# Kernel tuning notes

Hardware: AMD Instinct MI355X
Metric: run time of the kernel (lower is better)

Reference implementation:

```python
import jax, jax.numpy as jnp
import numpy as np

B, D, H1, H2 = 512, 1024, 512, 128

def setup_inputs() -> dict:
    key = jax.random.key(0)
    ks = jax.random.split(key, 3)
    x = jax.random.normal(ks[0], (B, D), dtype=jnp.float32)
    W1 = jax.random.normal(ks[1], (H1, D), dtype=jnp.float32)
    W2 = jax.random.normal(ks[2], (H2, H1), dtype=jnp.float32)
    b1 = jnp.full((H1,), 0.1, dtype=jnp.float32)
    b2 = jnp.full((H2,), 0.1, dtype=jnp.float32)
    b3 = jnp.full((H1,), 0.1, dtype=jnp.float32)
    b_r = jnp.full((D,), 0.1, dtype=jnp.float32)
    return {"x": x, "W1": W1, "b1": b1, "W2": W2, "b2": b2, "b3": b3, "b_r": b_r}

def reference(x, W1, b1, W2, b2, b3, b_r):
    # encoder
    c1 = jax.nn.sigmoid(x @ W1.T + b1)          # [B, H1]
    c2 = jax.nn.sigmoid(c1 @ W2.T + b2)         # [B, H2]
    # decoder (tied weights)
    c3 = jax.nn.sigmoid(c2 @ W2 + b3)           # [B, H1]
    recover = c3 @ W1 + b_r                     # [B, D]
    # Jacobian of code w.r.t. x, batched (replaces per-sample diag+matmul loop):
    # Jac[b] = diag(c2'(b)) @ W2 @ diag(c1'(b)) @ W1
    s1p = c1 * (1.0 - c1)                       # [B, H1]
    s2p = c2 * (1.0 - c2)                       # [B, H2]
    M = s2p[:, :, None] * W2[None, :, :] * s1p[:, None, :]   # [B, H2, H1]
    Jac = jnp.einsum('bhk,kd->bhd', M, W1)      # [B, H2, D]
    return (recover, c2, Jac)
```

## Files before the change

### kernel.cpp

```cpp
#include <hip/hip_runtime.h>


typedef _Float16 f16x8 __attribute__((ext_vector_type(8)));
typedef _Float16 f16x4 __attribute__((ext_vector_type(4)));
typedef float    f32x4 __attribute__((ext_vector_type(4)));
typedef float    f32x2 __attribute__((ext_vector_type(2)));

__device__ __forceinline__ void gld_lds16(const _Float16* src, _Float16* dst_wave_uniform) {
    __builtin_amdgcn_global_load_lds((const __attribute__((address_space(1))) unsigned int*)src,
                                     (__attribute__((address_space(3))) unsigned int*)dst_wave_uniform,
                                     16, 0, 0);
}

__device__ __forceinline__ void prep_dev(int bx, const float* __restrict__ W1,
                                         const float* __restrict__ W2,
                                         _Float16* __restrict__ W1T,
                                         _Float16* __restrict__ W2h) {
    if (bx < 512) {
        __shared__ float tile[32][33];
        int dt = (bx & 31) * 32, kt = (bx >> 5) * 32;
        int tx = threadIdx.x & 31, ty = threadIdx.x >> 5;
        #pragma unroll
        for (int r = 0; r < 32; r += 8)
            tile[ty + r][tx] = W1[(kt + ty + r) * 1024 + dt + tx];
        __syncthreads();
        #pragma unroll
        for (int r = 0; r < 32; r += 8)
            W1T[(size_t)(dt + ty + r) * 512 + kt + tx] = (_Float16)tile[tx][ty + r];
    } else {
        int i = (bx - 512) * 1024 + threadIdx.x * 4;
        f32x4 v = *(const f32x4*)(W2 + i);
        f16x4 h;
        h.x = (_Float16)v.x; h.y = (_Float16)v.y; h.z = (_Float16)v.z; h.w = (_Float16)v.w;
        *(f16x4*)(W2h + i) = h;
    }
}

template <int EPI, bool TRANSB>
__device__ void gemm_dev(const float* __restrict__ A, const float* __restrict__ Bm,
                         const float* __restrict__ bias,
                         float* __restrict__ C, float* __restrict__ Cd,
                         _Float16* __restrict__ Ch,
                         int M, int N, int K, int m0, int n0) {
    __shared__ __align__(16) float As[32][34];
    __shared__ __align__(16) float Bs[32][68];
    const int tid = threadIdx.x, tx = tid & 15, ty = tid >> 4;
    const int ka  = tid & 31, ma  = tid >> 5;
    const int kbt = tid & 31, nbt = tid >> 5;
    const int nbf = tid & 63, kbf = tid >> 6;
    float acc[2][4] = {};
    float rA[4], rB[8];

    #pragma unroll
    for (int r = 0; r < 4; ++r) rA[r] = A[(size_t)(m0 + ma + 8 * r) * K + ka];
    if (TRANSB) {
        #pragma unroll
        for (int r = 0; r < 8; ++r) rB[r] = Bm[(size_t)(n0 + nbt + 8 * r) * K + kbt];
    } else {
        #pragma unroll
        for (int r = 0; r < 8; ++r) rB[r] = Bm[(size_t)(kbf + 4 * r) * N + n0 + nbf];
    }

    for (int k0 = 0; k0 < K; k0 += 32) {
        #pragma unroll
        for (int r = 0; r < 4; ++r) As[ka][ma + 8 * r] = rA[r];
        if (TRANSB) {
            #pragma unroll
            for (int r = 0; r < 8; ++r) Bs[kbt][nbt + 8 * r] = rB[r];
        } else {
            #pragma unroll
            for (int r = 0; r < 8; ++r) Bs[kbf + 4 * r][nbf] = rB[r];
        }
        const int k1 = k0 + 32;
        if (k1 < K) {
            #pragma unroll
            for (int r = 0; r < 4; ++r) rA[r] = A[(size_t)(m0 + ma + 8 * r) * K + k1 + ka];
            if (TRANSB) {
                #pragma unroll
                for (int r = 0; r < 8; ++r) rB[r] = Bm[(size_t)(n0 + nbt + 8 * r) * K + k1 + kbt];
            } else {
                #pragma unroll
                for (int r = 0; r < 8; ++r) rB[r] = Bm[(size_t)(k1 + kbf + 4 * r) * N + n0 + nbf];
            }
        }
        __syncthreads();
        #pragma unroll
        for (int k = 0; k < 32; ++k) {
            f32x2 av = *(const f32x2*)&As[k][ty * 2];
            f32x4 bv = *(const f32x4*)&Bs[k][tx * 4];
            #pragma unroll
            for (int i = 0; i < 2; ++i)
                #pragma unroll
                for (int j = 0; j < 4; ++j)
                    acc[i][j] += av[i] * bv[j];
        }
        __syncthreads();
    }

    #pragma unroll
    for (int i = 0; i < 2; ++i) {
        int row = m0 + ty * 2 + i;
        #pragma unroll
        for (int j = 0; j < 4; ++j) {
            int col = n0 + tx * 4 + j;
            float z = acc[i][j] + bias[col];
            float s = 1.f / (1.f + __expf(-z));
            if constexpr (EPI == 1) {
                C[(size_t)row * N + col]  = s;
                Cd[(size_t)row * N + col] = s * (1.f - s);
            } else {
                Ch[(size_t)row * N + col] = (_Float16)s;
            }
        }
    }
}

__global__ __launch_bounds__(256) void fused_prep_gemm1(const float* __restrict__ x,
                                                        const float* __restrict__ W1,
                                                        const float* __restrict__ b1,
                                                        const float* __restrict__ W2,
                                                        _Float16* __restrict__ W1T,
                                                        _Float16* __restrict__ W2h,
                                                        float* __restrict__ c1,
                                                        float* __restrict__ s1p) {
    int bx = blockIdx.x;
    if (bx < 128) {
        gemm_dev<1, true>(x, W1, b1, c1, s1p, nullptr, 512, 512, 1024,
                          (bx >> 3) * 32, (bx & 7) * 64);
    } else {
        prep_dev(bx - 128, W1, W2, W1T, W2h);
    }
}

__global__ __launch_bounds__(256) void gemm2_kernel(const float* __restrict__ c1,
                                                    const float* __restrict__ W2,
                                                    const float* __restrict__ b2,
                                                    float* __restrict__ out_c2,
                                                    float* __restrict__ s2p) {
    gemm_dev<1, true>(c1, W2, b2, out_c2, s2p, nullptr, 512, 128, 512,
                      blockIdx.y * 32, blockIdx.x * 64);
}

__global__ __launch_bounds__(256) void gemm3_kernel(const float* __restrict__ out_c2,
                                                    const float* __restrict__ W2,
                                                    const float* __restrict__ b3,
                                                    _Float16* __restrict__ c3h) {
    gemm_dev<2, false>(out_c2, W2, b3, nullptr, nullptr, c3h, 512, 512, 128,
                       (blockIdx.x >> 3) * 32, (blockIdx.x & 7) * 64);
}

__global__ __launch_bounds__(256, 2) void jacW_fused(const _Float16* __restrict__ c3h,
                                                     const _Float16* __restrict__ W2h,
                                                     const _Float16* __restrict__ W1T,
                                                     const float* __restrict__ s1p,
                                                     const float* __restrict__ s2p,
                                                     const float* __restrict__ br,
                                                     float* __restrict__ out_rec,
                                                     float* __restrict__ out_jac) {
    __shared__ __align__(16) _Float16 Wsl[128 * 64];
    __shared__ __align__(16) _Float16 Bsl[128 * 64];
    __shared__ _Float16 S1h[2][512];
    __shared__ float    S2s[2][128];

    const int tid = threadIdx.x;
    const int lane = tid & 63, wave = tid >> 6;
    const int wm = (wave >> 1) * 64, wn = (wave & 1) * 64;
    const int l15 = lane & 15, q = lane >> 4;
    const int bid = blockIdx.x;

    const int srow = wave * 8 + (lane >> 3);
    const int skof = ((lane & 7) ^ (lane >> 3)) * 8;

    if (bid < 32) {
        const int m0 = (bid >> 3) * 128, n0 = (bid & 7) * 128;
        const _Float16* Abase = c3h + (size_t)m0 * 512;
        const _Float16* Bbase = W1T + (size_t)n0 * 512;
        float* outp = out_rec + (size_t)m0 * 1024;
        if (tid < 128) S2s[0][tid] = br[n0 + tid];

        f32x4 acc[4][4];
        #pragma unroll
        for (int i = 0; i < 4; ++i)
            #pragma unroll
            for (int j = 0; j < 4; ++j) acc[i][j] = (f32x4){0.f, 0.f, 0.f, 0.f};

        for (int t = 0; t < 8; ++t) {
            const int kb = t * 64;
            #pragma unroll
            for (int r = 0; r < 4; ++r) {
                gld_lds16(Abase + (size_t)(r * 32 + srow) * 512 + kb + skof, Wsl + (r * 32 + wave * 8) * 64);
                gld_lds16(Bbase + (size_t)(r * 32 + srow) * 512 + kb + skof, Bsl + (r * 32 + wave * 8) * 64);
            }
            __syncthreads();
            #pragma unroll
            for (int kk = 0; kk < 64; kk += 32) {
                f16x8 af[4], bf[4];
                #pragma unroll
                for (int i = 0; i < 4; ++i)
                    af[i] = *(const f16x8*)(Wsl + (wm + i * 16 + l15) * 64 + ((kk + q * 8) ^ ((l15 & 7) * 8)));
                #pragma unroll
                for (int j = 0; j < 4; ++j)
                    bf[j] = *(const f16x8*)(Bsl + (wn + j * 16 + l15) * 64 + ((kk + q * 8) ^ ((l15 & 7) * 8)));
                #pragma unroll
                for (int i = 0; i < 4; ++i)
                    #pragma unroll
                    for (int j = 0; j < 4; ++j)
                        acc[i][j] = __builtin_amdgcn_mfma_f32_16x16x32_f16(af[i], bf[j], acc[i][j], 0, 0, 0);
            }
            __syncthreads();
        }

        #pragma unroll
        for (int i = 0; i < 4; ++i) {
            #pragma unroll
            for (int rg = 0; rg < 4; ++rg) {
                int ml = wm + i * 16 + q * 4 + rg;
                #pragma unroll
                for (int j = 0; j < 4; ++j) {
                    int cl = wn + j * 16 + l15;
                    __builtin_nontemporal_store(acc[i][j][rg] + S2s[0][cl],
                                                outp + (size_t)ml * 1024 + n0 + cl);
                }
            }
        }
        return;
    }

    const int jid = bid - 32;
    const int w = (jid & 7) * 256 + (jid >> 3);
    const int pair = w >> 3, n0 = (w & 7) * 128;
    const int bA = pair * 2;

    S1h[0][tid]       = (_Float16)s1p[(size_t)bA * 512 + tid];
    S1h[0][tid + 256] = (_Float16)s1p[(size_t)bA * 512 + 256 + tid];
    S1h[1][tid]       = (_Float16)s1p[(size_t)(bA + 1) * 512 + tid];
    S1h[1][tid + 256] = (_Float16)s1p[(size_t)(bA + 1) * 512 + 256 + tid];
    if (tid < 128) S2s[0][tid] = s2p[(size_t)bA * 128 + tid];
    else           S2s[1][tid - 128] = s2p[(size_t)(bA + 1) * 128 + (tid - 128)];

    const _Float16* Bbase = W1T + (size_t)n0 * 512;

    f32x4 accA[4][4], accB[4][4];
    #pragma unroll
    for (int i = 0; i < 4; ++i)
        #pragma unroll
        for (int j = 0; j < 4; ++j) {
            accA[i][j] = (f32x4){0.f, 0.f, 0.f, 0.f};
            accB[i][j] = (f32x4){0.f, 0.f, 0.f, 0.f};
        }

    for (int t = 0; t < 8; ++t) {
        const int kb = t * 64;
        #pragma unroll
        for (int r = 0; r < 4; ++r) {
            gld_lds16(W2h   + (size_t)(r * 32 + srow) * 512 + kb + skof, Wsl + (r * 32 + wave * 8) * 64);
            gld_lds16(Bbase + (size_t)(r * 32 + srow) * 512 + kb + skof, Bsl + (r * 32 + wave * 8) * 64);
        }
        __syncthreads();
        #pragma unroll
        for (int kk = 0; kk < 64; kk += 32) {
            const f16x8 sfA = *(const f16x8*)(&S1h[0][kb + kk + q * 8]);
            const f16x8 sfB = *(const f16x8*)(&S1h[1][kb + kk + q * 8]);
            f16x8 bf[4];
            #pragma unroll
            for (int j = 0; j < 4; ++j)
                bf[j] = *(const f16x8*)(Bsl + (wn + j * 16 + l15) * 64 + ((kk + q * 8) ^ ((l15 & 7) * 8)));
            #pragma unroll
            for (int i = 0; i < 4; ++i) {
                const f16x8 wf = *(const f16x8*)(Wsl + (wm + i * 16 + l15) * 64 + ((kk + q * 8) ^ ((l15 & 7) * 8)));
                f16x8 af = wf * sfA;
                #pragma unroll
                for (int j = 0; j < 4; ++j)
                    accA[i][j] = __builtin_amdgcn_mfma_f32_16x16x32_f16(af, bf[j], accA[i][j], 0, 0, 0);
                af = wf * sfB;
                #pragma unroll
                for (int j = 0; j < 4; ++j)
                    accB[i][j] = __builtin_amdgcn_mfma_f32_16x16x32_f16(af, bf[j], accB[i][j], 0, 0, 0);
            }
        }
        __syncthreads();
    }

    float* outA = out_jac + (size_t)bA * (128 * 1024);
    float* outB = outA + (128 * 1024);
    #pragma unroll
    for (int i = 0; i < 4; ++i) {
        #pragma unroll
        for (int rg = 0; rg < 4; ++rg) {
            int ml = wm + i * 16 + q * 4 + rg;
            float rsA = S2s[0][ml], rsB = S2s[1][ml];
            #pragma unroll
            for (int j = 0; j < 4; ++j) {
                int cl = wn + j * 16 + l15;
                __builtin_nontemporal_store(accA[i][j][rg] * rsA, outA + (size_t)ml * 1024 + n0 + cl);
                __builtin_nontemporal_store(accB[i][j][rg] * rsB, outB + (size_t)ml * 1024 + n0 + cl);
            }
        }
    }
}

extern "C" void kernel_launch(void* const* d_in, const int* in_sizes, int n_in,
                              void* d_out, int out_size, void* d_ws, size_t ws_size,
                              hipStream_t stream) {
    const float* x  = (const float*)d_in[0];
    const float* W1 = (const float*)d_in[1];
    const float* b1 = (const float*)d_in[2];
    const float* W2 = (const float*)d_in[3];
    const float* b2 = (const float*)d_in[4];
    const float* b3 = (const float*)d_in[5];
    const float* br = (const float*)d_in[6];

    float* out_rec = (float*)d_out;
    float* out_c2  = out_rec + 512 * 1024;
    float* out_jac = out_c2 + 512 * 128;

    char* ws = (char*)d_ws;
    _Float16* W1T = (_Float16*)(ws);
    _Float16* W2h = (_Float16*)(ws + 0x100000);
    float*    c1  = (float*)(ws + 0x120000);
    float*    s1p = (float*)(ws + 0x220000);
    float*    s2p = (float*)(ws + 0x320000);
    _Float16* c3h = (_Float16*)(ws + 0x360000);

    fused_prep_gemm1<<<704, 256, 0, stream>>>(x, W1, b1, W2, W1T, W2h, c1, s1p);
    gemm2_kernel<<<dim3(2, 16), 256, 0, stream>>>(c1, W2, b2, out_c2, s2p);
    gemm3_kernel<<<128, 256, 0, stream>>>(out_c2, W2, b3, c3h);
    jacW_fused<<<2080, 256, 0, stream>>>(c3h, W2h, W1T, s1p, s2p, br, out_rec, out_jac);
}
```

Baseline: 404.3 us.

## Split paired-sample Jacobian GEMM into two passes, overlapping first sample's stores

The Jacobian block previously computed both samples of a pair in one K loop and stored everything at the end. Now it computes sample A fully, then streams sample A's output stores in slices interleaved with sample B's K-loop iterations, so global writes overlap MFMA work. The cost is loading the W2 and W1T tiles into LDS twice (once per sample) and full unrolling of both loops, which increases code size and may change register pressure.

New measurement: 435.1 us. +7.6%, slower.

```diff
diff --git a/kernel.cpp b/kernel.cpp
--- a/kernel.cpp
+++ b/kernel.cpp
@@ -239,6 +239,8 @@
     else           S2s[1][tid - 128] = s2p[(size_t)(bA + 1) * 128 + (tid - 128)];
 
     const _Float16* Bbase = W1T + (size_t)n0 * 512;
+    float* outA = out_jac + (size_t)bA * (128 * 1024);
+    float* outB = outA + (128 * 1024);
 
     f32x4 accA[4][4], accB[4][4];
     #pragma unroll
@@ -249,6 +251,7 @@
             accB[i][j] = (f32x4){0.f, 0.f, 0.f, 0.f};
         }
 
+    #pragma unroll
     for (int t = 0; t < 8; ++t) {
         const int kb = t * 64;
         #pragma unroll
@@ -260,6 +263,48 @@
         #pragma unroll
         for (int kk = 0; kk < 64; kk += 32) {
             const f16x8 sfA = *(const f16x8*)(&S1h[0][kb + kk + q * 8]);
+            f16x8 bf[4];
+            #pragma unroll
+            for (int j = 0; j < 4; ++j)
+                bf[j] = *(const f16x8*)(Bsl + (wn + j * 16 + l15) * 64 + ((kk + q * 8) ^ ((l15 & 7) * 8)));
+            #pragma unroll
+            for (int i = 0; i < 4; ++i) {
+                const f16x8 wf = *(const f16x8*)(Wsl + (wm + i * 16 + l15) * 64 + ((kk + q * 8) ^ ((l15 & 7) * 8)));
+                const f16x8 af = wf * sfA;
+                #pragma unroll
+                for (int j = 0; j < 4; ++j)
+                    accA[i][j] = __builtin_amdgcn_mfma_f32_16x16x32_f16(af, bf[j], accA[i][j], 0, 0, 0);
+            }
+        }
+        __syncthreads();
+    }
+
+    #pragma unroll
+    for (int t = 0; t < 8; ++t) {
+        const int kb = t * 64;
+        #pragma unroll
+        for (int r = 0; r < 4; ++r) {
+            gld_lds16(W2h   + (size_t)(r * 32 + srow) * 512 + kb + skof, Wsl + (r * 32 + wave * 8) * 64);
+            gld_lds16(Bbase + (size_t)(r * 32 + srow) * 512 + kb + skof, Bsl + (r * 32 + wave * 8) * 64);
+        }
+        {
+            const int i = t >> 1;
+            #pragma unroll
+            for (int r2 = 0; r2 < 2; ++r2) {
+                const int rg = (t & 1) * 2 + r2;
+                const int ml = wm + i * 16 + q * 4 + rg;
+                const float rs = S2s[0][ml];
+                #pragma unroll
+                for (int j = 0; j < 4; ++j) {
+                    const int cl = wn + j * 16 + l15;
+                    __builtin_nontemporal_store(accA[i][j][rg] * rs,
+                                                outA + (size_t)ml * 1024 + n0 + cl);
+                }
+            }
+        }
+        __syncthreads();
+        #pragma unroll
+        for (int kk = 0; kk < 64; kk += 32) {
             const f16x8 sfB = *(const f16x8*)(&S1h[1][kb + kk + q * 8]);
             f16x8 bf[4];
             #pragma unroll
@@ -268,11 +313,7 @@
             #pragma unroll
             for (int i = 0; i < 4; ++i) {
                 const f16x8 wf = *(const f16x8*)(Wsl + (wm + i * 16 + l15) * 64 + ((kk + q * 8) ^ ((l15 & 7) * 8)));
-                f16x8 af = wf * sfA;
-                #pragma unroll
-                for (int j = 0; j < 4; ++j)
-                    accA[i][j] = __builtin_amdgcn_mfma_f32_16x16x32_f16(af, bf[j], accA[i][j], 0, 0, 0);
-                af = wf * sfB;
+                const f16x8 af = wf * sfB;
                 #pragma unroll
                 for (int j = 0; j < 4; ++j)
                     accB[i][j] = __builtin_amdgcn_mfma_f32_16x16x32_f16(af, bf[j], accB[i][j], 0, 0, 0);
@@ -281,19 +322,17 @@
         __syncthreads();
     }
 
-    float* outA = out_jac + (size_t)bA * (128 * 1024);
-    float* outB = outA + (128 * 1024);
     #pragma unroll
     for (int i = 0; i < 4; ++i) {
         #pragma unroll
         for (int rg = 0; rg < 4; ++rg) {
-            int ml = wm + i * 16 + q * 4 + rg;
-            float rsA = S2s[0][ml], rsB = S2s[1][ml];
+            const int ml = wm + i * 16 + q * 4 + rg;
+            const float rs = S2s[1][ml];
             #pragma unroll
             for (int j = 0; j < 4; ++j) {
-                int cl = wn + j * 16 + l15;
-                __builtin_nontemporal_store(accA[i][j][rg] * rsA, outA + (size_t)ml * 1024 + n0 + cl);
-                __builtin_nontemporal_store(accB[i][j][rg] * rsB, outB + (size_t)ml * 1024 + n0 + cl);
+                const int cl = wn + j * 16 + l15;
+                __builtin_nontemporal_store(accB[i][j][rg] * rs,
+                                            outB + (size_t)ml * 1024 + n0 + cl);
             }
         }
     }
```

## Merge four launches into one cooperative persistent kernel with grid syncs

Applied to the files above, without the earlier changes.

Replaces the four separate kernel launches with a single cooperative mega-kernel of 512 blocks that runs prep/GEMM1, GEMM2, GEMM3 and the Jacobian/recover phase separated by grid-wide syncs, with a persistent loop over the 2080 final-phase work units. The goal is to remove launch gaps and inter-kernel drain/fill overhead. The cost is grid.sync latency, fixed 512-block occupancy (launch bounds of 2 blocks per CU), loss of the earlier interleaved jac work ordering for L2 reuse, and the early GEMM phases running on few blocks. Falls back to the old path if cooperative launch fails.

After: 574.5 us. +42.1%, slower.

```diff
diff --git a/kernel.cpp b/kernel.cpp
--- a/kernel.cpp
+++ b/kernel.cpp
@@ -1,4 +1,7 @@
 #include <hip/hip_runtime.h>
+#include <hip/hip_cooperative_groups.h>
+
+namespace cg = cooperative_groups;
 
 
 typedef _Float16 f16x8 __attribute__((ext_vector_type(8)));
@@ -20,6 +23,7 @@
         __shared__ float tile[32][33];
         int dt = (bx & 31) * 32, kt = (bx >> 5) * 32;
         int tx = threadIdx.x & 31, ty = threadIdx.x >> 5;
+        __syncthreads();
         #pragma unroll
         for (int r = 0; r < 32; r += 8)
             tile[ty + r][tx] = W1[(kt + ty + r) * 1024 + dt + tx];
@@ -115,6 +119,206 @@
     }
 }
 
+__device__ __forceinline__ void unit_guard() {
+    asm volatile("s_waitcnt lgkmcnt(0)" ::: "memory");
+    __builtin_amdgcn_sched_barrier(0);
+    __builtin_amdgcn_s_barrier();
+}
+
+__device__ __forceinline__ void recover_unit(int u,
+        _Float16* __restrict__ Wsl, _Float16* __restrict__ Bsl, float* __restrict__ S2s0,
+        const _Float16* __restrict__ c3h, const _Float16* __restrict__ W1T,
+        const float* __restrict__ br, float* __restrict__ out_rec) {
+    const int tid = threadIdx.x;
+    const int lane = tid & 63, wave = tid >> 6;
+    const int wm = (wave >> 1) * 64, wn = (wave & 1) * 64;
+    const int l15 = lane & 15, q = lane >> 4;
+    const int srow = wave * 8 + (lane >> 3);
+    const int skof = ((lane & 7) ^ (lane >> 3)) * 8;
+
+    unit_guard();
+
+    const int m0 = (u >> 3) * 128, n0 = (u & 7) * 128;
+    const _Float16* Abase = c3h + (size_t)m0 * 512;
+    const _Float16* Bbase = W1T + (size_t)n0 * 512;
+    float* outp = out_rec + (size_t)m0 * 1024;
+    if (tid < 128) S2s0[tid] = br[n0 + tid];
+
+    f32x4 acc[4][4];
+    #pragma unroll
+    for (int i = 0; i < 4; ++i)
+        #pragma unroll
+        for (int j = 0; j < 4; ++j) acc[i][j] = (f32x4){0.f, 0.f, 0.f, 0.f};
+
+    for (int t = 0; t < 8; ++t) {
+        const int kb = t * 64;
+        #pragma unroll
+        for (int r = 0; r < 4; ++r) {
+            gld_lds16(Abase + (size_t)(r * 32 + srow) * 512 + kb + skof, Wsl + (r * 32 + wave * 8) * 64);
+            gld_lds16(Bbase + (size_t)(r * 32 + srow) * 512 + kb + skof, Bsl + (r * 32 + wave * 8) * 64);
+        }
+        __syncthreads();
+        #pragma unroll
+        for (int kk = 0; kk < 64; kk += 32) {
+            f16x8 af[4], bf[4];
+            #pragma unroll
+            for (int i = 0; i < 4; ++i)
+                af[i] = *(const f16x8*)(Wsl + (wm + i * 16 + l15) * 64 + ((kk + q * 8) ^ ((l15 & 7) * 8)));
+            #pragma unroll
+            for (int j = 0; j < 4; ++j)
+                bf[j] = *(const f16x8*)(Bsl + (wn + j * 16 + l15) * 64 + ((kk + q * 8) ^ ((l15 & 7) * 8)));
+            #pragma unroll
+            for (int i = 0; i < 4; ++i)
+                #pragma unroll
+                for (int j = 0; j < 4; ++j)
+                    acc[i][j] = __builtin_amdgcn_mfma_f32_16x16x32_f16(af[i], bf[j], acc[i][j], 0, 0, 0);
+        }
+        __syncthreads();
+    }
+
+    #pragma unroll
+    for (int i = 0; i < 4; ++i) {
+        #pragma unroll
+        for (int rg = 0; rg < 4; ++rg) {
+            int ml = wm + i * 16 + q * 4 + rg;
+            #pragma unroll
+            for (int j = 0; j < 4; ++j) {
+                int cl = wn + j * 16 + l15;
+                __builtin_nontemporal_store(acc[i][j][rg] + S2s0[cl],
+                                            outp + (size_t)ml * 1024 + n0 + cl);
+            }
+        }
+    }
+}
+
+__device__ __forceinline__ void jac_unit(int jid,
+        _Float16* __restrict__ Wsl, _Float16* __restrict__ Bsl,
+        _Float16 (*__restrict__ S1h)[512], float (*__restrict__ S2s)[128],
+        const _Float16* __restrict__ W2h, const _Float16* __restrict__ W1T,
+        const float* __restrict__ s1p, const float* __restrict__ s2p,
+        float* __restrict__ out_jac) {
+    const int tid = threadIdx.x;
+    const int lane = tid & 63, wave = tid >> 6;
+    const int wm = (wave >> 1) * 64, wn = (wave & 1) * 64;
+    const int l15 = lane & 15, q = lane >> 4;
+    const int srow = wave * 8 + (lane >> 3);
+    const int skof = ((lane & 7) ^ (lane >> 3)) * 8;
+
+    unit_guard();
+
+    const int pair = jid >> 3, n0 = (jid & 7) * 128;
+    const int bA = pair * 2;
+
+    S1h[0][tid]       = (_Float16)s1p[(size_t)bA * 512 + tid];
+    S1h[0][tid + 256] = (_Float16)s1p[(size_t)bA * 512 + 256 + tid];
+    S1h[1][tid]       = (_Float16)s1p[(size_t)(bA + 1) * 512 + tid];
+    S1h[1][tid + 256] = (_Float16)s1p[(size_t)(bA + 1) * 512 + 256 + tid];
+    if (tid < 128) S2s[0][tid] = s2p[(size_t)bA * 128 + tid];
+    else           S2s[1][tid - 128] = s2p[(size_t)(bA + 1) * 128 + (tid - 128)];
+
+    const _Float16* Bbase = W1T + (size_t)n0 * 512;
+
+    f32x4 accA[4][4], accB[4][4];
+    #pragma unroll
+    for (int i = 0; i < 4; ++i)
+        #pragma unroll
+        for (int j = 0; j < 4; ++j) {
+            accA[i][j] = (f32x4){0.f, 0.f, 0.f, 0.f};
+            accB[i][j] = (f32x4){0.f, 0.f, 0.f, 0.f};
+        }
+
+    for (int t = 0; t < 8; ++t) {
+        const int kb = t * 64;
+        #pragma unroll
+        for (int r = 0; r < 4; ++r) {
+            gld_lds16(W2h   + (size_t)(r * 32 + srow) * 512 + kb + skof, Wsl + (r * 32 + wave * 8) * 64);
+            gld_lds16(Bbase + (size_t)(r * 32 + srow) * 512 + kb + skof, Bsl + (r * 32 + wave * 8) * 64);
+        }
+        __syncthreads();
+        #pragma unroll
+        for (int kk = 0; kk < 64; kk += 32) {
+            const f16x8 sfA = *(const f16x8*)(&S1h[0][kb + kk + q * 8]);
+            const f16x8 sfB = *(const f16x8*)(&S1h[1][kb + kk + q * 8]);
+            f16x8 bf[4];
+            #pragma unroll
+            for (int j = 0; j < 4; ++j)
+                bf[j] = *(const f16x8*)(Bsl + (wn + j * 16 + l15) * 64 + ((kk + q * 8) ^ ((l15 & 7) * 8)));
+            #pragma unroll
+            for (int i = 0; i < 4; ++i) {
+                const f16x8 wf = *(const f16x8*)(Wsl + (wm + i * 16 + l15) * 64 + ((kk + q * 8) ^ ((l15 & 7) * 8)));
+                f16x8 af = wf * sfA;
+                #pragma unroll
+                for (int j = 0; j < 4; ++j)
+                    accA[i][j] = __builtin_amdgcn_mfma_f32_16x16x32_f16(af, bf[j], accA[i][j], 0, 0, 0);
+                af = wf * sfB;
+                #pragma unroll
+                for (int j = 0; j < 4; ++j)
+                    accB[i][j] = __builtin_amdgcn_mfma_f32_16x16x32_f16(af, bf[j], accB[i][j], 0, 0, 0);
+            }
+        }
+        __syncthreads();
+    }
+
+    float* outA = out_jac + (size_t)bA * (128 * 1024);
+    float* outB = outA + (128 * 1024);
+    #pragma unroll
+    for (int i = 0; i < 4; ++i) {
+        #pragma unroll
+        for (int rg = 0; rg < 4; ++rg) {
+            int ml = wm + i * 16 + q * 4 + rg;
+            float rsA = S2s[0][ml], rsB = S2s[1][ml];
+            #pragma unroll
+            for (int j = 0; j < 4; ++j) {
+                int cl = wn + j * 16 + l15;
+                __builtin_nontemporal_store(accA[i][j][rg] * rsA, outA + (size_t)ml * 1024 + n0 + cl);
+                __builtin_nontemporal_store(accB[i][j][rg] * rsB, outB + (size_t)ml * 1024 + n0 + cl);
+            }
+        }
+    }
+}
+
+__global__ __launch_bounds__(256, 2) void mega_kernel(
+        const float* __restrict__ x,  const float* __restrict__ W1, const float* __restrict__ b1,
+        const float* __restrict__ W2, const float* __restrict__ b2, const float* __restrict__ b3,
+        const float* __restrict__ br,
+        _Float16* __restrict__ W1T, _Float16* __restrict__ W2h,
+        float* __restrict__ c1, float* __restrict__ s1p, float* __restrict__ s2p,
+        _Float16* __restrict__ c3h,
+        float* __restrict__ out_rec, float* __restrict__ out_c2, float* __restrict__ out_jac) {
+    __shared__ __align__(16) _Float16 Wsl[128 * 64];
+    __shared__ __align__(16) _Float16 Bsl[128 * 64];
+    __shared__ _Float16 S1h[2][512];
+    __shared__ float    S2s[2][128];
+
+    cg::grid_group grid = cg::this_grid();
+    const int bid = blockIdx.x;
+
+    if (bid < 128) {
+        gemm_dev<1, true>(x, W1, b1, c1, s1p, nullptr, 512, 512, 1024,
+                          (bid >> 3) * 32, (bid & 7) * 64);
+    } else {
+        int u = bid - 128;
+        prep_dev(u, W1, W2, W1T, W2h);
+        if (u + 384 < 576) prep_dev(u + 384, W1, W2, W1T, W2h);
+    }
+    grid.sync();
+
+    if (bid < 32)
+        gemm_dev<1, true>(c1, W2, b2, out_c2, s2p, nullptr, 512, 128, 512,
+                          (bid >> 1) * 32, (bid & 1) * 64);
+    grid.sync();
+
+    if (bid < 128)
+        gemm_dev<2, false>(out_c2, W2, b3, nullptr, nullptr, c3h, 512, 512, 128,
+                           (bid >> 3) * 32, (bid & 7) * 64);
+    grid.sync();
+
+    for (int u = bid; u < 2080; u += 512) {
+        if (u < 32) recover_unit(u, Wsl, Bsl, S2s[0], c3h, W1T, br, out_rec);
+        else        jac_unit(u - 32, Wsl, Bsl, S1h, S2s, W2h, W1T, s1p, s2p, out_jac);
+    }
+}
+
 __global__ __launch_bounds__(256) void fused_prep_gemm1(const float* __restrict__ x,
                                                         const float* __restrict__ W1,
                                                         const float* __restrict__ b1,
@@ -162,141 +366,14 @@
     __shared__ _Float16 S1h[2][512];
     __shared__ float    S2s[2][128];
 
-    const int tid = threadIdx.x;
-    const int lane = tid & 63, wave = tid >> 6;
-    const int wm = (wave >> 1) * 64, wn = (wave & 1) * 64;
-    const int l15 = lane & 15, q = lane >> 4;
     const int bid = blockIdx.x;
-
-    const int srow = wave * 8 + (lane >> 3);
-    const int skof = ((lane & 7) ^ (lane >> 3)) * 8;
-
     if (bid < 32) {
-        const int m0 = (bid >> 3) * 128, n0 = (bid & 7) * 128;
-        const _Float16* Abase = c3h + (size_t)m0 * 512;
-        const _Float16* Bbase = W1T + (size_t)n0 * 512;
-        float* outp = out_rec + (size_t)m0 * 1024;
-        if (tid < 128) S2s[0][tid] = br[n0 + tid];
-
-        f32x4 acc[4][4];
-        #pragma unroll
-        for (int i = 0; i < 4; ++i)
-            #pragma unroll
-            for (int j = 0; j < 4; ++j) acc[i][j] = (f32x4){0.f, 0.f, 0.f, 0.f};
-
-        for (int t = 0; t < 8; ++t) {
-            const int kb = t * 64;
-            #pragma unroll
-            for (int r = 0; r < 4; ++r) {
-                gld_lds16(Abase + (size_t)(r * 32 + srow) * 512 + kb + skof, Wsl + (r * 32 + wave * 8) * 64);
-                gld_lds16(Bbase + (size_t)(r * 32 + srow) * 512 + kb + skof, Bsl + (r * 32 + wave * 8) * 64);
-            }
-            __syncthreads();
-            #pragma unroll
-            for (int kk = 0; kk < 64; kk += 32) {
-                f16x8 af[4], bf[4];
-                #pragma unroll
-                for (int i = 0; i < 4; ++i)
-                    af[i] = *(const f16x8*)(Wsl + (wm + i * 16 + l15) * 64 + ((kk + q * 8) ^ ((l15 & 7) * 8)));
-                #pragma unroll
-                for (int j = 0; j < 4; ++j)
-                    bf[j] = *(const f16x8*)(Bsl + (wn + j * 16 + l15) * 64 + ((kk + q * 8) ^ ((l15 & 7) * 8)));
-                #pragma unroll
-                for (int i = 0; i < 4; ++i)
-                    #pragma unroll
-                    for (int j = 0; j < 4; ++j)
-                        acc[i][j] = __builtin_amdgcn_mfma_f32_16x16x32_f16(af[i], bf[j], acc[i][j], 0, 0, 0);
-            }
-            __syncthreads();
-        }
-
-        #pragma unroll
-        for (int i = 0; i < 4; ++i) {
-            #pragma unroll
-            for (int rg = 0; rg < 4; ++rg) {
-                int ml = wm + i * 16 + q * 4 + rg;
-                #pragma unroll
-                for (int j = 0; j < 4; ++j) {
-                    int cl = wn + j * 16 + l15;
-                    __builtin_nontemporal_store(acc[i][j][rg] + S2s[0][cl],
-                                                outp + (size_t)ml * 1024 + n0 + cl);
-                }
-            }
-        }
+        recover_unit(bid, Wsl, Bsl, S2s[0], c3h, W1T, br, out_rec);
         return;
     }
-
     const int jid = bid - 32;
     const int w = (jid & 7) * 256 + (jid >> 3);
-    const int pair = w >> 3, n0 = (w & 7) * 128;
-    const int bA = pair * 2;
-
-    S1h[0][tid]       = (_Float16)s1p[(size_t)bA * 512 + tid];
-    S1h[0][tid + 256] = (_Float16)s1p[(size_t)bA * 512 + 256 + tid];
-    S1h[1][tid]       = (_Float16)s1p[(size_t)(bA + 1) * 512 + tid];
-    S1h[1][tid + 256] = (_Float16)s1p[(size_t)(bA + 1) * 512 + 256 + tid];
-    if (tid < 128) S2s[0][tid] = s2p[(size_t)bA * 128 + tid];
-    else           S2s[1][tid - 128] = s2p[(size_t)(bA + 1) * 128 + (tid - 128)];
-
-    const _Float16* Bbase = W1T + (size_t)n0 * 512;
-
-    f32x4 accA[4][4], accB[4][4];
-    #pragma unroll
-    for (int i = 0; i < 4; ++i)
-        #pragma unroll
-        for (int j = 0; j < 4; ++j) {
-            accA[i][j] = (f32x4){0.f, 0.f, 0.f, 0.f};
-            accB[i][j] = (f32x4){0.f, 0.f, 0.f, 0.f};
-        }
-
-    for (int t = 0; t < 8; ++t) {
-        const int kb = t * 64;
-        #pragma unroll
-        for (int r = 0; r < 4; ++r) {
-            gld_lds16(W2h   + (size_t)(r * 32 + srow) * 512 + kb + skof, Wsl + (r * 32 + wave * 8) * 64);
-            gld_lds16(Bbase + (size_t)(r * 32 + srow) * 512 + kb + skof, Bsl + (r * 32 + wave * 8) * 64);
-        }
-        __syncthreads();
-        #pragma unroll
-        for (int kk = 0; kk < 64; kk += 32) {
-            const f16x8 sfA = *(const f16x8*)(&S1h[0][kb + kk + q * 8]);
-            const f16x8 sfB = *(const f16x8*)(&S1h[1][kb + kk + q * 8]);
-            f16x8 bf[4];
-            #pragma unroll
-            for (int j = 0; j < 4; ++j)
-                bf[j] = *(const f16x8*)(Bsl + (wn + j * 16 + l15) * 64 + ((kk + q * 8) ^ ((l15 & 7) * 8)));
-            #pragma unroll
-            for (int i = 0; i < 4; ++i) {
-                const f16x8 wf = *(const f16x8*)(Wsl + (wm + i * 16 + l15) * 64 + ((kk + q * 8) ^ ((l15 & 7) * 8)));
-                f16x8 af = wf * sfA;
-                #pragma unroll
-                for (int j = 0; j < 4; ++j)
-                    accA[i][j] = __builtin_amdgcn_mfma_f32_16x16x32_f16(af, bf[j], accA[i][j], 0, 0, 0);
-                af = wf * sfB;
-                #pragma unroll
-                for (int j = 0; j < 4; ++j)
-                    accB[i][j] = __builtin_amdgcn_mfma_f32_16x16x32_f16(af, bf[j], accB[i][j], 0, 0, 0);
-            }
-        }
-        __syncthreads();
-    }
-
-    float* outA = out_jac + (size_t)bA * (128 * 1024);
-    float* outB = outA + (128 * 1024);
-    #pragma unroll
-    for (int i = 0; i < 4; ++i) {
-        #pragma unroll
-        for (int rg = 0; rg < 4; ++rg) {
-            int ml = wm + i * 16 + q * 4 + rg;
-            float rsA = S2s[0][ml], rsB = S2s[1][ml];
-            #pragma unroll
-            for (int j = 0; j < 4; ++j) {
-                int cl = wn + j * 16 + l15;
-                __builtin_nontemporal_store(accA[i][j][rg] * rsA, outA + (size_t)ml * 1024 + n0 + cl);
-                __builtin_nontemporal_store(accB[i][j][rg] * rsB, outB + (size_t)ml * 1024 + n0 + cl);
-            }
-        }
-    }
+    jac_unit(w, Wsl, Bsl, S1h, S2s, W2h, W1T, s1p, s2p, out_jac);
 }
 
 extern "C" void kernel_launch(void* const* d_in, const int* in_sizes, int n_in,
@@ -322,8 +399,24 @@
     float*    s2p = (float*)(ws + 0x320000);
     _Float16* c3h = (_Float16*)(ws + 0x360000);
 
-    fused_prep_gemm1<<<704, 256, 0, stream>>>(x, W1, b1, W2, W1T, W2h, c1, s1p);
-    gemm2_kernel<<<dim3(2, 16), 256, 0, stream>>>(c1, W2, b2, out_c2, s2p);
-    gemm3_kernel<<<128, 256, 0, stream>>>(out_c2, W2, b3, c3h);
-    jacW_fused<<<2080, 256, 0, stream>>>(c3h, W2h, W1T, s1p, s2p, br, out_rec, out_jac);
-}
+    int dev = 0, coop = 0;
+    hipGetDevice(&dev);
+    hipDeviceGetAttribute(&coop, hipDeviceAttributeCooperativeLaunch, dev);
+
+    hipError_t lerr = hipErrorUnknown;
+    if (coop) {
+        void* args[] = {(void*)&x, (void*)&W1, (void*)&b1, (void*)&W2, (void*)&b2,
+                        (void*)&b3, (void*)&br, (void*)&W1T, (void*)&W2h, (void*)&c1,
+                        (void*)&s1p, (void*)&s2p, (void*)&c3h,
+                        (void*)&out_rec, (void*)&out_c2, (void*)&out_jac};
+        lerr = hipLaunchCooperativeKernel((const void*)mega_kernel, dim3(512), dim3(256),
+                                          args, 0, stream);
+    }
+    if (lerr != hipSuccess) {
+        (void)hipGetLastError();
+        fused_prep_gemm1<<<704, 256, 0, stream>>>(x, W1, b1, W2, W1T, W2h, c1, s1p);
+        gemm2_kernel<<<dim3(2, 16), 256, 0, stream>>>(c1, W2, b2, out_c2, s2p);
+        gemm3_kernel<<<128, 256, 0, stream>>>(out_c2, W2, b3, c3h);
+        jacW_fused<<<2080, 256, 0, stream>>>(c3h, W2h, W1T, s1p, s2p, br, out_rec, out_jac);
+    }
+}
```
